# Optimization experiments

Hardware: AMD Instinct MI355X
Metric: run time of the kernel (lower is better)

Reference implementation:

```python
import jax, jax.numpy as jnp
import numpy as np

B, S, D, H = 2, 2048, 1024, 16
DK = D // H

def setup_inputs() -> dict:
    key = jax.random.key(0)
    k_x, k_q, k_k, k_v, k_o = jax.random.split(key, 5)
    return {
        "x": jax.random.normal(k_x, (B, S, D), dtype=jnp.float32),
        "wq": jax.random.normal(k_q, (D, D), dtype=jnp.float32) * 0.02,
        "wk": jax.random.normal(k_k, (D, D), dtype=jnp.float32) * 0.02,
        "wv": jax.random.normal(k_v, (D, D), dtype=jnp.float32) * 0.02,
        "wo": jax.random.normal(k_o, (D, D), dtype=jnp.float32) * 0.02,
    }

def reference(x, wq, wk, wv, wo):
    b, s, d = x.shape
    # project and split heads: [b, h, s, dk]
    q = (x @ wq).reshape(b, s, H, DK).transpose(0, 2, 1, 3)
    k = (x @ wk).reshape(b, s, H, DK).transpose(0, 2, 1, 3)
    v = (x @ wv).reshape(b, s, H, DK).transpose(0, 2, 1, 3)
    scores = jnp.einsum("bhqd,bhkd->bhqk", q, k) / jnp.sqrt(jnp.float32(DK))
    causal = jnp.tril(jnp.ones((s, s), dtype=bool))  # True = keep
    scores = jnp.where(causal, scores, jnp.finfo(scores.dtype).min)
    probs = jax.nn.softmax(scores, axis=-1)  # dropout pdrop=0.0 -> identity
    out = jnp.einsum("bhqk,bhkd->bhqd", probs, v)
    out = out.transpose(0, 2, 1, 3).reshape(b, s, d)
    return out @ wo
```

## Files before the change

### kernel.cpp

```cpp
#include <hip/hip_runtime.h>
#include <hip/hip_bf16.h>

typedef short s16x8 __attribute__((ext_vector_type(8)));
typedef float f32x4 __attribute__((ext_vector_type(4)));
typedef float f32x16 __attribute__((ext_vector_type(16)));
typedef unsigned short u16x4 __attribute__((ext_vector_type(4)));
typedef unsigned int u32x4 __attribute__((ext_vector_type(4)));

#define D_MODEL 1024
#define N_HEAD  16
#define D_HEAD  64
#define SEQ     2048
#define NBATCH  2

#if __has_builtin(__builtin_amdgcn_exp2f)
#define EXP2(x) __builtin_amdgcn_exp2f(x)
#else
#define EXP2(x) exp2f(x)
#endif

#define GLOAD_LDS16(g, l) \
    __builtin_amdgcn_global_load_lds((const __attribute__((address_space(1))) void*)(g), \
                                     (__attribute__((address_space(3))) void*)(l), 16, 0, 0)

__device__ __forceinline__ unsigned short f2bf(float f) {
    union { float f; unsigned int u; } v; v.f = f;
    unsigned int r = v.u + 0x7FFFu + ((v.u >> 16) & 1u);
    return (unsigned short)(r >> 16);
}

__device__ __forceinline__ unsigned cvtpk_bf16(float lo, float hi) {
    unsigned r;
    asm("v_cvt_pk_bf16_f32 %0, %1, %2" : "=v"(r) : "v"(lo), "v"(hi));
    return r;
}


__global__ __launch_bounds__(256) void cvt_x_kernel(const float* __restrict__ in,
                                                    unsigned short* __restrict__ out) {
    int i = (blockIdx.x * 256 + threadIdx.x) * 4;
    float4 v = *reinterpret_cast<const float4*>(in + i);
    u16x4 o;
    o.x = f2bf(v.x); o.y = f2bf(v.y); o.z = f2bf(v.z); o.w = f2bf(v.w);
    *reinterpret_cast<u16x4*>(out + i) = o;
}

__global__ __launch_bounds__(256) void cvt_w_kernel(
    const float* __restrict__ w0, const float* __restrict__ w1,
    const float* __restrict__ w2, const float* __restrict__ w3,
    unsigned short* __restrict__ o0, unsigned short* __restrict__ o1,
    unsigned short* __restrict__ o2, unsigned short* __restrict__ o3)
{
    __shared__ unsigned short T[64][72];
    const int t = threadIdx.x;
    const int z = blockIdx.y;
    const float* w = (z == 0) ? w0 : (z == 1) ? w1 : (z == 2) ? w2 : w3;
    unsigned short* wt = (z == 0) ? o0 : (z == 1) ? o1 : (z == 2) ? o2 : o3;
    const int k0 = ((int)blockIdx.x & 15) * 64, n0 = ((int)blockIdx.x >> 4) * 64;
#pragma unroll
    for (int i = 0; i < 4; ++i) {
        int k = (t >> 4) + i * 16;
        int n = (t & 15) * 4;
        float4 v = *reinterpret_cast<const float4*>(&w[(k0 + k) * 1024 + n0 + n]);
        T[n + 0][k] = f2bf(v.x); T[n + 1][k] = f2bf(v.y);
        T[n + 2][k] = f2bf(v.z); T[n + 3][k] = f2bf(v.w);
    }
    __syncthreads();
#pragma unroll
    for (int i = 0; i < 2; ++i) {
        int n = (t >> 3) + i * 32;
        int kc = (t & 7) * 8;
        *reinterpret_cast<s16x8*>(&wt[(n0 + n) * 1024 + k0 + kc]) =
            *reinterpret_cast<const s16x8*>(&T[n][kc]);
    }
}


__global__ __launch_bounds__(256, 3) void gemm_qkv_kernel(
    const unsigned short* __restrict__ xb,
    const unsigned short* __restrict__ wqt, const unsigned short* __restrict__ wkt,
    const unsigned short* __restrict__ wvt,
    unsigned short* __restrict__ Qb, unsigned short* __restrict__ Kb,
    unsigned short* __restrict__ Vtb)
{
    __shared__ unsigned short As[128 * 64];
    __shared__ unsigned short Bs[128 * 64];
    const int t = threadIdx.x, lane = t & 63, wid = t >> 6;
    const int wr = wid >> 1, wc = wid & 1;
    const int l15 = lane & 15, l4 = lane >> 4;
    const int m0 = blockIdx.y * 128, n0 = blockIdx.x * 128;
    const int z = blockIdx.z;
    const unsigned short* Bt = (z == 0) ? wqt : (z == 1) ? wkt : wvt;

    const int srow = t >> 3;
    const int srcoff = (((t & 7) ^ (srow & 7)) << 3);
    const unsigned short* Ab = xb + (size_t)(m0 + srow) * D_MODEL + srcoff;
    const unsigned short* Bb = Bt + (size_t)(n0 + srow) * D_MODEL + srcoff;
    const int ldsoff = t * 8;
    const int rsw = l15 & 7;

    f32x4 acc[4][4];
#pragma unroll
    for (int m = 0; m < 4; ++m)
#pragma unroll
        for (int n = 0; n < 4; ++n) acc[m][n] = (f32x4){0.f, 0.f, 0.f, 0.f};

    for (int k0 = 0; k0 < D_MODEL; k0 += 64) {
        __syncthreads();
#pragma unroll
        for (int i = 0; i < 4; ++i) {
            GLOAD_LDS16(Ab + (size_t)(i * 32) * D_MODEL + k0, &As[i * 2048 + ldsoff]);
            GLOAD_LDS16(Bb + (size_t)(i * 32) * D_MODEL + k0, &Bs[i * 2048 + ldsoff]);
        }
        __syncthreads();

#pragma unroll
        for (int ks = 0; ks < 2; ++ks) {
            const int csl = ks * 4 + l4;
            s16x8 af[4], bfr[4];
#pragma unroll
            for (int m = 0; m < 4; ++m)
                af[m] = *reinterpret_cast<const s16x8*>(
                    &As[(wr * 64 + m * 16 + l15) * 64 + ((csl ^ rsw) << 3)]);
#pragma unroll
            for (int n = 0; n < 4; ++n)
                bfr[n] = *reinterpret_cast<const s16x8*>(
                    &Bs[(wc * 64 + n * 16 + l15) * 64 + ((csl ^ rsw) << 3)]);
            __builtin_amdgcn_s_setprio(1);
#pragma unroll
            for (int m = 0; m < 4; ++m)
#pragma unroll
                for (int n = 0; n < 4; ++n)
                    acc[m][n] = __builtin_amdgcn_mfma_f32_16x16x32_bf16(af[m], bfr[n], acc[m][n], 0, 0, 0);
            __builtin_amdgcn_s_setprio(0);
        }
    }

    const int rb = m0 + wr * 64, cb = n0 + wc * 64;
    if (z == 2) {
#pragma unroll
        for (int m = 0; m < 4; ++m) {
            int row = rb + m * 16 + l4 * 4;
            int b = row >> 11, s = row & 2047;
#pragma unroll
            for (int n = 0; n < 4; ++n) {
                int col = cb + n * 16 + l15;
                int h = col >> 6, dk = col & 63;
                u16x4 o;
                o.x = f2bf(acc[m][n][0]); o.y = f2bf(acc[m][n][1]);
                o.z = f2bf(acc[m][n][2]); o.w = f2bf(acc[m][n][3]);
                *reinterpret_cast<u16x4*>(&Vtb[(((b * N_HEAD + h) * D_HEAD + dk) << 11) + s]) = o;
            }
        }
    } else {
        unsigned short* C = (z == 0) ? Qb : Kb;
        const float alpha = (z == 0) ? 0.18033688011112042f : 1.0f;
#pragma unroll
        for (int m = 0; m < 4; ++m)
#pragma unroll
            for (int n = 0; n < 4; ++n)
#pragma unroll
                for (int r = 0; r < 4; ++r)
                    C[(rb + m * 16 + l4 * 4 + r) * D_MODEL + cb + n * 16 + l15] =
                        f2bf(acc[m][n][r] * alpha);
    }
}


__global__ __launch_bounds__(256, 3) void gemm_out_kernel(
    const unsigned short* __restrict__ attnb, const unsigned short* __restrict__ wot,
    float* __restrict__ out)
{
    __shared__ unsigned short As[128 * 64];
    __shared__ unsigned short Bs[64 * 64];
    const int t = threadIdx.x, lane = t & 63, wid = t >> 6;
    const int wr = wid >> 1, wc = wid & 1;
    const int l15 = lane & 15, l4 = lane >> 4;
    const int m0 = blockIdx.y * 128, n0 = blockIdx.x * 64;

    const int srow = t >> 3;
    const int srcoff = (((t & 7) ^ (srow & 7)) << 3);
    const unsigned short* Ab = attnb + (size_t)(m0 + srow) * D_MODEL + srcoff;
    const unsigned short* Bb = wot + (size_t)(n0 + srow) * D_MODEL + srcoff;
    const int ldsoff = t * 8;
    const int rsw = l15 & 7;

    f32x4 acc[4][2];
#pragma unroll
    for (int m = 0; m < 4; ++m)
#pragma unroll
        for (int n = 0; n < 2; ++n) acc[m][n] = (f32x4){0.f, 0.f, 0.f, 0.f};

    for (int k0 = 0; k0 < D_MODEL; k0 += 64) {
        __syncthreads();
#pragma unroll
        for (int i = 0; i < 4; ++i)
            GLOAD_LDS16(Ab + (size_t)(i * 32) * D_MODEL + k0, &As[i * 2048 + ldsoff]);
#pragma unroll
        for (int i = 0; i < 2; ++i)
            GLOAD_LDS16(Bb + (size_t)(i * 32) * D_MODEL + k0, &Bs[i * 2048 + ldsoff]);
        __syncthreads();

#pragma unroll
        for (int ks = 0; ks < 2; ++ks) {
            const int csl = ks * 4 + l4;
            s16x8 af[4], bfr[2];
#pragma unroll
            for (int m = 0; m < 4; ++m)
                af[m] = *reinterpret_cast<const s16x8*>(
                    &As[(wr * 64 + m * 16 + l15) * 64 + ((csl ^ rsw) << 3)]);
#pragma unroll
            for (int n = 0; n < 2; ++n)
                bfr[n] = *reinterpret_cast<const s16x8*>(
                    &Bs[(wc * 32 + n * 16 + l15) * 64 + ((csl ^ rsw) << 3)]);
            __builtin_amdgcn_s_setprio(1);
#pragma unroll
            for (int m = 0; m < 4; ++m)
#pragma unroll
                for (int n = 0; n < 2; ++n)
                    acc[m][n] = __builtin_amdgcn_mfma_f32_16x16x32_bf16(af[m], bfr[n], acc[m][n], 0, 0, 0);
            __builtin_amdgcn_s_setprio(0);
        }
    }

    const int rb = m0 + wr * 64, cb = n0 + wc * 32;
#pragma unroll
    for (int m = 0; m < 4; ++m)
#pragma unroll
        for (int n = 0; n < 2; ++n)
#pragma unroll
            for (int r = 0; r < 4; ++r)
                out[(rb + m * 16 + l4 * 4 + r) * D_MODEL + cb + n * 16 + l15] = acc[m][n][r];
}


__global__ __launch_bounds__(128, 4) void attn_kernel(
    const unsigned short* __restrict__ Qb, const unsigned short* __restrict__ Kb,
    const unsigned short* __restrict__ Vtb, unsigned short* __restrict__ Ob)
{
    __shared__ unsigned short Ks[2][64 * 64];
    __shared__ unsigned short Vs[2][64 * 64];

    const int t = threadIdx.x;
    const int lane = t & 63, wid = t >> 6;
    const int l31 = lane & 31, l5 = lane >> 5;
    const int bh = blockIdx.y, b = bh >> 4, h = bh & 15;
    const int q0 = ((int)gridDim.x - 1 - (int)blockIdx.x) * 64;
    const int qw = q0 + wid * 32;
    const int qrow = qw + l31;

    s16x8 qf[4];
#pragma unroll
    for (int ks = 0; ks < 4; ++ks)
        qf[ks] = *reinterpret_cast<const s16x8*>(
            &Qb[(size_t)(b * SEQ + qrow) * D_MODEL + h * D_HEAD + ks * 16 + l5 * 8]);

    f32x16 oacc[2];
#pragma unroll
    for (int d = 0; d < 2; ++d)
#pragma unroll
        for (int r = 0; r < 16; ++r) oacc[d][r] = 0.f;
    float lrun = 0.f;

    const int srow = lane >> 3;
    const int scol = ((lane & 7) ^ srow) * 8;
    const unsigned short* kgb = Kb + (size_t)(b * SEQ + srow) * D_MODEL + h * D_HEAD + scol;
    const unsigned short* vgb = Vtb + ((size_t)(bh * D_HEAD + srow) << 11) + scol;
    const int swz = (l31 & 7);

#define STAGE(bufidx, kvbase) do { \
    if (wid == 0) { \
        const unsigned short* kg = kgb + (size_t)(kvbase) * D_MODEL; \
        _Pragma("unroll") \
        for (int i_ = 0; i_ < 8; ++i_) \
            GLOAD_LDS16(kg + (size_t)(i_ * 8) * D_MODEL, &Ks[bufidx][i_ * 512]); \
    } else { \
        const unsigned short* vg = vgb + (kvbase); \
        _Pragma("unroll") \
        for (int i_ = 0; i_ < 8; ++i_) \
            GLOAD_LDS16(vg + ((size_t)(i_ * 8) << 11), &Vs[bufidx][i_ * 512]); \
    } } while (0)

    const int ntiles = (q0 >> 6) + 1;
    STAGE(0, 0);

    for (int ti = 0; ti < ntiles; ++ti) {
        const int cur = ti & 1;
        const int kv0 = ti * 64;
        __builtin_amdgcn_sched_barrier(0);
        asm volatile("s_waitcnt vmcnt(0)" ::: "memory");
        __builtin_amdgcn_s_barrier();
        if (ti + 1 < ntiles) STAGE(cur ^ 1, kv0 + 64);
        __builtin_amdgcn_sched_barrier(0);

        const unsigned short* KsC = &Ks[cur][0];
        const unsigned short* VsC = &Vs[cur][0];

        f32x16 sacc[2];
#pragma unroll
        for (int kvsub = 0; kvsub < 2; ++kvsub) {
            const bool active = (kv0 + kvsub * 32 <= qw + 31);
            if (active) {
#pragma unroll
                for (int r = 0; r < 16; ++r) sacc[kvsub][r] = -8.0f;
                __builtin_amdgcn_s_setprio(1);
#pragma unroll
                for (int ks = 0; ks < 4; ++ks) {
                    s16x8 kf = *reinterpret_cast<const s16x8*>(
                        &KsC[(kvsub * 32 + l31) * 64 + (((2 * ks + l5) ^ swz) * 8)]);
                    sacc[kvsub] = __builtin_amdgcn_mfma_f32_32x32x16_bf16(kf, qf[ks], sacc[kvsub], 0, 0, 0);
                }
                __builtin_amdgcn_s_setprio(0);
                if (kv0 + kvsub * 32 + 31 > qw) {
                    int kvbase = kv0 + kvsub * 32 + 4 * l5;
#pragma unroll
                    for (int r = 0; r < 16; ++r) {
                        int kvg = kvbase + (r & 3) + 8 * (r >> 2);
                        sacc[kvsub][r] = (kvg > qrow) ? -1e30f : sacc[kvsub][r];
                    }
                }
#pragma unroll
                for (int r = 0; r < 16; ++r) sacc[kvsub][r] = EXP2(sacc[kvsub][r]);
            } else {
#pragma unroll
                for (int r = 0; r < 16; ++r) sacc[kvsub][r] = 0.f;
            }
        }

        float sred[16];
#pragma unroll
        for (int r = 0; r < 16; ++r) sred[r] = sacc[0][r] + sacc[1][r];
#pragma unroll
        for (int s = 8; s >= 1; s >>= 1)
#pragma unroll
            for (int r = 0; r < 8; ++r)
                if (r < s) sred[r] += sred[r + s];
        lrun += sred[0] + __shfl_xor(sred[0], 32);

#pragma unroll
        for (int ks = 0; ks < 4; ++ks) {
            if (kv0 + (ks >> 1) * 32 > qw + 31) continue;
            const int kvsub = ks >> 1, bo = (ks & 1) * 8;
            unsigned a0 = cvtpk_bf16(sacc[kvsub][bo + 0], sacc[kvsub][bo + 1]);
            unsigned a1 = cvtpk_bf16(sacc[kvsub][bo + 2], sacc[kvsub][bo + 3]);
            unsigned a2 = cvtpk_bf16(sacc[kvsub][bo + 4], sacc[kvsub][bo + 5]);
            unsigned a3 = cvtpk_bf16(sacc[kvsub][bo + 6], sacc[kvsub][bo + 7]);
            asm volatile("v_permlane32_swap_b32 %0, %1" : "+v"(a0), "+v"(a2));
            asm volatile("v_permlane32_swap_b32 %0, %1" : "+v"(a1), "+v"(a3));
            u32x4 pw; pw.x = a0; pw.y = a1; pw.z = a2; pw.w = a3;
            s16x8 pf = __builtin_bit_cast(s16x8, pw);
            __builtin_amdgcn_s_setprio(1);
#pragma unroll
            for (int dsub = 0; dsub < 2; ++dsub) {
                s16x8 vf = *reinterpret_cast<const s16x8*>(
                    &VsC[(dsub * 32 + l31) * 64 + (((2 * ks + l5) ^ swz) * 8)]);
                oacc[dsub] = __builtin_amdgcn_mfma_f32_32x32x16_bf16(vf, pf, oacc[dsub], 0, 0, 0);
            }
            __builtin_amdgcn_s_setprio(0);
        }
    }
    __syncthreads();

    unsigned short* Tr = &Ks[0][0];
    float inv = 1.f / lrun;
    const int orow = wid * 32 + l31;
#pragma unroll
    for (int dsub = 0; dsub < 2; ++dsub)
#pragma unroll
        for (int a = 0; a < 4; ++a) {
            unsigned w0 = cvtpk_bf16(oacc[dsub][4 * a + 0] * inv, oacc[dsub][4 * a + 1] * inv);
            unsigned w1 = cvtpk_bf16(oacc[dsub][4 * a + 2] * inv, oacc[dsub][4 * a + 3] * inv);
            int slot = (4 * dsub + a) ^ (orow & 7);
            uint2 pr; pr.x = w0; pr.y = w1;
            *reinterpret_cast<uint2*>(&Tr[orow * 64 + slot * 8 + l5 * 4]) = pr;
        }
    __syncthreads();
#pragma unroll
    for (int i = 0; i < 4; ++i) {
        int s = i * 128 + t;
        int row = s >> 3, c16 = s & 7;
        int cs = (c16 ^ (row & 7)) * 8;
        s16x8 v = *reinterpret_cast<const s16x8*>(&Tr[row * 64 + cs]);
        *reinterpret_cast<s16x8*>(
            &Ob[(size_t)(b * SEQ + q0 + row) * D_MODEL + h * D_HEAD + c16 * 8]) = v;
    }
#undef STAGE
}


extern "C" void kernel_launch(void* const* d_in, const int* in_sizes, int n_in,
                              void* d_out, int out_size, void* d_ws, size_t ws_size,
                              hipStream_t stream) {
    (void)in_sizes; (void)n_in; (void)out_size; (void)ws_size;
    const float* x  = (const float*)d_in[0];
    const float* wq = (const float*)d_in[1];
    const float* wk = (const float*)d_in[2];
    const float* wv = (const float*)d_in[3];
    const float* wo = (const float*)d_in[4];
    float* out = (float*)d_out;

    char* ws = (char*)d_ws;
    unsigned short* xb  = (unsigned short*)(ws);
    unsigned short* wqt = (unsigned short*)(ws + (8u  << 20));
    unsigned short* wkt = (unsigned short*)(ws + (10u << 20));
    unsigned short* wvt = (unsigned short*)(ws + (12u << 20));
    unsigned short* wot = (unsigned short*)(ws + (14u << 20));
    unsigned short* Qb  = (unsigned short*)(ws + (16u << 20));
    unsigned short* Kb  = (unsigned short*)(ws + (24u << 20));
    unsigned short* Vtb = (unsigned short*)(ws + (32u << 20));
    unsigned short* Ob  = (unsigned short*)(ws + (40u << 20));

    hipLaunchKernelGGL(cvt_x_kernel, dim3(4096), dim3(256), 0, stream, x, xb);
    hipLaunchKernelGGL(cvt_w_kernel, dim3(256, 4), dim3(256), 0, stream,
                       wq, wk, wv, wo, wqt, wkt, wvt, wot);

    hipLaunchKernelGGL(gemm_qkv_kernel, dim3(8, 32, 3), dim3(256), 0, stream,
                       xb, wqt, wkt, wvt, Qb, Kb, Vtb);
    hipLaunchKernelGGL(attn_kernel, dim3(32, 32), dim3(128), 0, stream, Qb, Kb, Vtb, Ob);
    hipLaunchKernelGGL(gemm_out_kernel, dim3(16, 32), dim3(256), 0, stream, Ob, wot, out);
}
```

Measured before the change: 115.4 us.

## Enlarge attention blocks to 256 query rows sharing each staged K/V tile

Each attention workgroup now covers 256 query rows with 8 waves instead of 64 rows with 2 waves. All waves share the same double-buffered K/V tiles in LDS, and the tile loads are spread across the waves. The goal is to cut redundant K/V global traffic across blocks and spread the load-issue work. In exchange the grid is four times smaller and causal imbalance grows: waves past their causal range still take part in every barrier while doing no compute, and there is less parallelism to fill the GPU.

```diff
diff --git a/kernel.cpp b/kernel.cpp
--- a/kernel.cpp
+++ b/kernel.cpp
@@ -234,18 +234,17 @@
 }
 
 
-__global__ __launch_bounds__(128, 4) void attn_kernel(
+__global__ __launch_bounds__(512, 2) void attn_kernel(
     const unsigned short* __restrict__ Qb, const unsigned short* __restrict__ Kb,
     const unsigned short* __restrict__ Vtb, unsigned short* __restrict__ Ob)
 {
-    __shared__ unsigned short Ks[2][64 * 64];
-    __shared__ unsigned short Vs[2][64 * 64];
+    __shared__ unsigned short SMEM[16384];
 
     const int t = threadIdx.x;
     const int lane = t & 63, wid = t >> 6;
     const int l31 = lane & 31, l5 = lane >> 5;
     const int bh = blockIdx.y, b = bh >> 4, h = bh & 15;
-    const int q0 = ((int)gridDim.x - 1 - (int)blockIdx.x) * 64;
+    const int q0 = ((int)gridDim.x - 1 - (int)blockIdx.x) * 256;
     const int qw = q0 + wid * 32;
     const int qrow = qw + l31;
 
@@ -262,26 +261,25 @@
         for (int r = 0; r < 16; ++r) oacc[d][r] = 0.f;
     float lrun = 0.f;
 
+    const int wk = wid & 3;
     const int srow = lane >> 3;
     const int scol = ((lane & 7) ^ srow) * 8;
-    const unsigned short* kgb = Kb + (size_t)(b * SEQ + srow) * D_MODEL + h * D_HEAD + scol;
-    const unsigned short* vgb = Vtb + ((size_t)(bh * D_HEAD + srow) << 11) + scol;
+    const unsigned short* kgb = Kb + (size_t)(b * SEQ + wk * 16 + srow) * D_MODEL + h * D_HEAD + scol;
+    const unsigned short* vgb = Vtb + ((size_t)(bh * D_HEAD + wk * 16 + srow) << 11) + scol;
     const int swz = (l31 & 7);
 
 #define STAGE(bufidx, kvbase) do { \
-    if (wid == 0) { \
+    if (wid < 4) { \
         const unsigned short* kg = kgb + (size_t)(kvbase) * D_MODEL; \
-        _Pragma("unroll") \
-        for (int i_ = 0; i_ < 8; ++i_) \
-            GLOAD_LDS16(kg + (size_t)(i_ * 8) * D_MODEL, &Ks[bufidx][i_ * 512]); \
+        GLOAD_LDS16(kg,                         &SMEM[(bufidx) * 4096 + (wk * 16) * 64]); \
+        GLOAD_LDS16(kg + (size_t)8 * D_MODEL,   &SMEM[(bufidx) * 4096 + (wk * 16 + 8) * 64]); \
     } else { \
         const unsigned short* vg = vgb + (kvbase); \
-        _Pragma("unroll") \
-        for (int i_ = 0; i_ < 8; ++i_) \
-            GLOAD_LDS16(vg + ((size_t)(i_ * 8) << 11), &Vs[bufidx][i_ * 512]); \
+        GLOAD_LDS16(vg,                         &SMEM[8192 + (bufidx) * 4096 + (wk * 16) * 64]); \
+        GLOAD_LDS16(vg + ((size_t)8 << 11),     &SMEM[8192 + (bufidx) * 4096 + (wk * 16 + 8) * 64]); \
     } } while (0)
 
-    const int ntiles = (q0 >> 6) + 1;
+    const int ntiles = (q0 >> 6) + 4;
     STAGE(0, 0);
 
     for (int ti = 0; ti < ntiles; ++ti) {
@@ -293,8 +291,10 @@
         if (ti + 1 < ntiles) STAGE(cur ^ 1, kv0 + 64);
         __builtin_amdgcn_sched_barrier(0);
 
-        const unsigned short* KsC = &Ks[cur][0];
-        const unsigned short* VsC = &Vs[cur][0];
+        if (kv0 > qw + 31) continue;
+
+        const unsigned short* KsC = &SMEM[cur * 4096];
+        const unsigned short* VsC = &SMEM[8192 + cur * 4096];
 
         f32x16 sacc[2];
 #pragma unroll
@@ -361,7 +361,6 @@
     }
     __syncthreads();
 
-    unsigned short* Tr = &Ks[0][0];
     float inv = 1.f / lrun;
     const int orow = wid * 32 + l31;
 #pragma unroll
@@ -372,15 +371,15 @@
             unsigned w1 = cvtpk_bf16(oacc[dsub][4 * a + 2] * inv, oacc[dsub][4 * a + 3] * inv);
             int slot = (4 * dsub + a) ^ (orow & 7);
             uint2 pr; pr.x = w0; pr.y = w1;
-            *reinterpret_cast<uint2*>(&Tr[orow * 64 + slot * 8 + l5 * 4]) = pr;
+            *reinterpret_cast<uint2*>(&SMEM[orow * 64 + slot * 8 + l5 * 4]) = pr;
         }
     __syncthreads();
 #pragma unroll
     for (int i = 0; i < 4; ++i) {
-        int s = i * 128 + t;
+        int s = i * 512 + t;
         int row = s >> 3, c16 = s & 7;
         int cs = (c16 ^ (row & 7)) * 8;
-        s16x8 v = *reinterpret_cast<const s16x8*>(&Tr[row * 64 + cs]);
+        s16x8 v = *reinterpret_cast<const s16x8*>(&SMEM[row * 64 + cs]);
         *reinterpret_cast<s16x8*>(
             &Ob[(size_t)(b * SEQ + q0 + row) * D_MODEL + h * D_HEAD + c16 * 8]) = v;
     }
@@ -416,6 +415,6 @@
 
     hipLaunchKernelGGL(gemm_qkv_kernel, dim3(8, 32, 3), dim3(256), 0, stream,
                        xb, wqt, wkt, wvt, Qb, Kb, Vtb);
-    hipLaunchKernelGGL(attn_kernel, dim3(32, 32), dim3(128), 0, stream, Qb, Kb, Vtb, Ob);
+    hipLaunchKernelGGL(attn_kernel, dim3(8, 32), dim3(512), 0, stream, Qb, Kb, Vtb, Ob);
     hipLaunchKernelGGL(gemm_out_kernel, dim3(16, 32), dim3(256), 0, stream, Ob, wot, out);
 }
```

Result: faster. 110.0 us (-4.7%).
